# Kernel optimization log

Hardware: AMD Instinct MI355X
Metric: run time of the kernel (lower is better)

Reference implementation:

```python
import jax, jax.numpy as jnp
import numpy as np

K_NEIGS = 3
M_PROB = 1.0
EPS = 1e-12


def _gen_G_single(ft):
    """Build normalized hypergraph Laplacian G [N,N] from node coords ft [N,3].

    Mirrors construct_H_with_KNN (is_probH=True, m_prob=1) + generate_G_from_H
    from the HGNN reference code: per-center KNN hyperedges with probabilistic
    incidence exp(-d^2/(m_prob*avg_d)^2), then G = Dv^-1/2 H De^-1 H^T Dv^-1/2.
    """
    N = ft.shape[0]
    # squared pairwise Euclidean distances [N,N]
    sq_norm = jnp.sum(ft * ft, axis=1)
    sq = jnp.maximum(sq_norm[:, None] + sq_norm[None, :] - 2.0 * ft @ ft.T, 0.0)
    dist = jnp.sqrt(sq + EPS)
    avg_dis = jnp.mean(dist, axis=1)  # per-center mean distance [N]
    # K nearest neighbors per center (self is always included: sq[c,c]=0)
    neg_sq, idx = jax.lax.top_k(-sq, K_NEIGS)  # [N,K]
    # prob incidence: exp(-d^2 / (m_prob*avg)^2); neg_sq = -d^2
    vals = jnp.exp(neg_sq / (M_PROB * avg_dis[:, None]) ** 2)  # [N,K]
    # H[node, edge]: column c holds the K neighbors of center c
    H = jnp.zeros((N, N), ft.dtype).at[idx, jnp.arange(N)[:, None]].set(vals)
    de = jnp.sum(H, axis=0)              # edge degrees [N]
    dv = jnp.sum(H, axis=1)              # vertex degrees [N]
    inv_de = 1.0 / de
    dv2 = dv ** -0.5
    HW = H * inv_de[None, :]
    G = (dv2[:, None] * (HW @ H.T)) * dv2[None, :]
    return G


def reference(x, W1, b1, Wc, bc):
    # gen_G: per-batch hypergraph G [B,N,N]
    G = jax.vmap(_gen_G_single)(x)
    # HGNN_conv with both args = G: out = G @ (G @ W1 + b1)  -> [B,N,H1]
    f = jnp.matmul(G, jnp.matmul(G, W1) + b1)
    # max-pool over nodes, then classifier
    f = jnp.max(f, axis=1)               # [B,H1]
    return f @ Wc + bc                   # [B,class_num]


def setup_inputs() -> dict:
    key = jax.random.key(0)
    k1, k2, k3, k4, k5 = jax.random.split(key, 5)
    B, N, H1, C = 4, 2048, 128, 8
    x = jax.random.normal(k1, (B, N, 3), dtype=jnp.float32)
    W1 = jax.random.normal(k2, (N, H1), dtype=jnp.float32) / np.sqrt(N)
    b1 = jax.random.normal(k3, (H1,), dtype=jnp.float32) * 0.01
    Wc = jax.random.normal(k4, (H1, C), dtype=jnp.float32) / np.sqrt(H1)
    bc = jax.random.normal(k5, (C,), dtype=jnp.float32) * 0.01
    return {"x": x, "W1": W1, "b1": b1, "Wc": Wc, "bc": bc}
```

## Files before the change

kernel.cpp:

```cpp
#include <hip/hip_runtime.h>
#include <math.h>

#define NN 2048
#define BB 4
#define HD 128
#define CNUM 8
#define WPB 4
#define PCHUNK 64
#define NCHUNKS (NN / PCHUNK)

typedef unsigned long long u64;

__device__ __forceinline__ u64 pack_key(float sq, int j) {
    return ((u64)__float_as_uint(sq) << 32) | (unsigned)j;
}
__device__ __forceinline__ void ins3(u64 k, u64& k0, u64& k1, u64& k2) {
    u64 a = k  < k2 ? k  : k2;
    u64 b = k0 > a  ? k0 : a;
    k0    = k0 < a  ? k0 : a;
    k2    = k1 > b  ? k1 : b;
    k1    = k1 < b  ? k1 : b;
}

__global__ void k_prep(const float* __restrict__ x, float4* __restrict__ pts) {
    const int t = blockIdx.x * 256 + threadIdx.x;
    const float a = x[3 * t], c = x[3 * t + 1], d = x[3 * t + 2];
    pts[t] = make_float4(a, c, d, a * a + c * c + d * d);
}

__global__ __launch_bounds__(256) void k_dist(
        const float4* __restrict__ pts,
        int* __restrict__ idx, float* __restrict__ vals,
        float* __restrict__ de, float* __restrict__ dv) {
    const int b = blockIdx.y;
    const float4* pb = pts + b * NN;
    const int wave = threadIdx.x >> 6;
    const int lane = threadIdx.x & 63;
    const int i = blockIdx.x * WPB + wave;
    const float4 ci = pb[i];
    u64 k0 = ~0ull, k1 = ~0ull, k2 = ~0ull;
    float dsA = 0.f, dsB = 0.f;
    for (int t = lane; t < NN; t += 256) {
        const float4 pa = pb[t];
        const float4 pv = pb[t + 64];
        const float4 pc = pb[t + 128];
        const float4 pd = pb[t + 192];
        const float qa = fmaxf(ci.w + pa.w - 2.0f * (ci.x * pa.x + ci.y * pa.y + ci.z * pa.z), 0.0f);
        const float qb = fmaxf(ci.w + pv.w - 2.0f * (ci.x * pv.x + ci.y * pv.y + ci.z * pv.z), 0.0f);
        const float qc = fmaxf(ci.w + pc.w - 2.0f * (ci.x * pc.x + ci.y * pc.y + ci.z * pc.z), 0.0f);
        const float qd = fmaxf(ci.w + pd.w - 2.0f * (ci.x * pd.x + ci.y * pd.y + ci.z * pd.z), 0.0f);
        dsA += __builtin_amdgcn_sqrtf(qa + 1e-12f) + __builtin_amdgcn_sqrtf(qc + 1e-12f);
        dsB += __builtin_amdgcn_sqrtf(qb + 1e-12f) + __builtin_amdgcn_sqrtf(qd + 1e-12f);
        ins3(pack_key(qa, t),       k0, k1, k2);
        ins3(pack_key(qb, t + 64),  k0, k1, k2);
        ins3(pack_key(qc, t + 128), k0, k1, k2);
        ins3(pack_key(qd, t + 192), k0, k1, k2);
    }
    float dsum = dsA + dsB;
    for (int off = 32; off > 0; off >>= 1) {
        const u64 o0 = __shfl_xor(k0, off);
        const u64 o1 = __shfl_xor(k1, off);
        const u64 o2 = __shfl_xor(k2, off);
        dsum += __shfl_xor(dsum, off);
        ins3(o0, k0, k1, k2);
        ins3(o1, k0, k1, k2);
        ins3(o2, k0, k1, k2);
    }
    if (lane == 0) {
        const float s0 = __uint_as_float((unsigned)(k0 >> 32));
        const float s1 = __uint_as_float((unsigned)(k1 >> 32));
        const float s2 = __uint_as_float((unsigned)(k2 >> 32));
        const int   i0 = (int)(k0 & 0xffffffffu);
        const int   i1 = (int)(k1 & 0xffffffffu);
        const int   i2 = (int)(k2 & 0xffffffffu);
        const float avg = dsum * (1.0f / NN);
        const float inva2 = 1.0f / (avg * avg);
        const float v0 = expf(-s0 * inva2);
        const float v1 = expf(-s1 * inva2);
        const float v2 = expf(-s2 * inva2);
        const int base = (b * NN + i) * 3;
        idx[base] = i0; idx[base + 1] = i1; idx[base + 2] = i2;
        vals[base] = v0; vals[base + 1] = v1; vals[base + 2] = v2;
        de[b * NN + i] = v0 + v1 + v2;
        atomicAdd(&dv[b * NN + i0], v0);
        atomicAdd(&dv[b * NN + i1], v1);
        atomicAdd(&dv[b * NN + i2], v2);
    }
}

__global__ void k_conv1(const float* __restrict__ W1, const int* __restrict__ idx,
                        const float* __restrict__ vals, const float* __restrict__ de,
                        const float* __restrict__ dv, float* __restrict__ Z1) {
    const int e = blockIdx.x * 2 + (threadIdx.x >> 7);
    const int b = blockIdx.y, h = threadIdx.x & (HD - 1);
    const int base = (b * NN + e) * 3;
    const int j0 = idx[base], j1 = idx[base + 1], j2 = idx[base + 2];
    const float v0 = vals[base], v1 = vals[base + 1], v2 = vals[base + 2];
    const float ide = 1.0f / de[b * NN + e];
    const float g0 = v0 * rsqrtf(dv[b * NN + j0]);
    const float g1 = v1 * rsqrtf(dv[b * NN + j1]);
    const float g2 = v2 * rsqrtf(dv[b * NN + j2]);
    const float y = ide * (g0 * W1[j0 * HD + h] + g1 * W1[j1 * HD + h] + g2 * W1[j2 * HD + h]);
    atomicAdd(&Z1[((size_t)(b * NN + j0)) * HD + h], v0 * y);
    atomicAdd(&Z1[((size_t)(b * NN + j1)) * HD + h], v1 * y);
    atomicAdd(&Z1[((size_t)(b * NN + j2)) * HD + h], v2 * y);
}

__global__ void k_conv2(const float* __restrict__ b1, const int* __restrict__ idx,
                        const float* __restrict__ vals, const float* __restrict__ de,
                        const float* __restrict__ dv, const float* __restrict__ Z1,
                        float* __restrict__ Z2) {
    const int e = blockIdx.x * 2 + (threadIdx.x >> 7);
    const int b = blockIdx.y, h = threadIdx.x & (HD - 1);
    const int base = (b * NN + e) * 3;
    const int j0 = idx[base], j1 = idx[base + 1], j2 = idx[base + 2];
    const float v0 = vals[base], v1 = vals[base + 1], v2 = vals[base + 2];
    const float ide = 1.0f / de[b * NN + e];
    const float bh = b1[h];
    const float d0 = rsqrtf(dv[b * NN + j0]);
    const float d1 = rsqrtf(dv[b * NN + j1]);
    const float d2 = rsqrtf(dv[b * NN + j2]);
    const float f0 = d0 * Z1[((size_t)(b * NN + j0)) * HD + h] + bh;
    const float f1 = d1 * Z1[((size_t)(b * NN + j1)) * HD + h] + bh;
    const float f2 = d2 * Z1[((size_t)(b * NN + j2)) * HD + h] + bh;
    const float y = ide * (v0 * d0 * f0 + v1 * d1 * f1 + v2 * d2 * f2);
    atomicAdd(&Z2[((size_t)(b * NN + j0)) * HD + h], v0 * y);
    atomicAdd(&Z2[((size_t)(b * NN + j1)) * HD + h], v1 * y);
    atomicAdd(&Z2[((size_t)(b * NN + j2)) * HD + h], v2 * y);
}

__global__ void k_pool1(const float* __restrict__ dv, const float* __restrict__ Z2,
                        float* __restrict__ pmax) {
    const int b = blockIdx.x, ch = blockIdx.y, h = threadIdx.x;
    const int v0 = ch * PCHUNK;
    float mx = -INFINITY;
    for (int v = v0; v < v0 + PCHUNK; ++v) {
        const float d2 = rsqrtf(dv[b * NN + v]);
        mx = fmaxf(mx, d2 * Z2[((size_t)(b * NN + v)) * HD + h]);
    }
    pmax[(b * NCHUNKS + ch) * HD + h] = mx;
}

__global__ void k_pool2(const float* __restrict__ Wc, const float* __restrict__ bc,
                        const float* __restrict__ pmax, float* __restrict__ out) {
    __shared__ float smax[HD];
    const int b = blockIdx.x, h = threadIdx.x;
    float mx = -INFINITY;
    for (int c = 0; c < NCHUNKS; ++c)
        mx = fmaxf(mx, pmax[(b * NCHUNKS + c) * HD + h]);
    smax[h] = mx;
    __syncthreads();
    if (h < CNUM) {
        float acc = bc[h];
        for (int q = 0; q < HD; ++q) acc += smax[q] * Wc[q * CNUM + h];
        out[b * CNUM + h] = acc;
    }
}

extern "C" void kernel_launch(void* const* d_in, const int* in_sizes, int n_in,
                              void* d_out, int out_size, void* d_ws, size_t ws_size,
                              hipStream_t stream) {
    const float* x  = (const float*)d_in[0];
    const float* W1 = (const float*)d_in[1];
    const float* b1 = (const float*)d_in[2];
    const float* Wc = (const float*)d_in[3];
    const float* bc = (const float*)d_in[4];
    float* out = (float*)d_out;

    float* ws = (float*)d_ws;
    float* dv   = ws;
    float* Z1   = dv + BB * NN;
    float* Z2   = Z1 + (size_t)BB * NN * HD;
    float* vals = Z2 + (size_t)BB * NN * HD;
    float* de   = vals + BB * NN * 3;
    int*   idx  = (int*)(de + BB * NN);
    float* pmax = (float*)(idx + BB * NN * 3);
    float4* pts = (float4*)(pmax + BB * NCHUNKS * HD);

    hipMemsetAsync(dv, 0, (size_t)(BB * NN) * (1 + 2 * HD) * sizeof(float), stream);

    k_prep<<<BB * NN / 256, 256, 0, stream>>>(x, pts);
    k_dist<<<dim3(NN / WPB, BB), 256, 0, stream>>>(pts, idx, vals, de, dv);
    k_conv1<<<dim3(NN / 2, BB), 256, 0, stream>>>(W1, idx, vals, de, dv, Z1);
    k_conv2<<<dim3(NN / 2, BB), 256, 0, stream>>>(b1, idx, vals, de, dv, Z1, Z2);
    k_pool1<<<dim3(BB, NCHUNKS), HD, 0, stream>>>(dv, Z2, pmax);
    k_pool2<<<BB, HD, 0, stream>>>(Wc, bc, pmax, out);
}
```

Measured before the change: 119.3 us.

## Replace scatter atomics with CSR gather for hypergraph convolutions

Builds a per-batch CSR incidence list (node to hyperedges) with a prefix scan and shared-memory cursors in a new k_csr kernel. Each convolution is split into an edge pass that writes per-edge features and a node pass that gathers them through the CSR, so the large float atomicAdd scatters into Z1/Z2 go away. The 8 MB memset of Z1/Z2 also goes away, and dv^-1/2 is precomputed once. In exchange it adds three kernel launches and a CSR build that runs on only four blocks, and the order in which each node's contributions are summed is no longer fixed.

```diff
diff --git a/kernel.cpp b/kernel.cpp
--- a/kernel.cpp
+++ b/kernel.cpp
@@ -31,7 +31,7 @@
 __global__ __launch_bounds__(256) void k_dist(
         const float4* __restrict__ pts,
         int* __restrict__ idx, float* __restrict__ vals,
-        float* __restrict__ de, float* __restrict__ dv) {
+        float* __restrict__ de, float* __restrict__ dv, int* __restrict__ ecnt) {
     const int b = blockIdx.y;
     const float4* pb = pts + b * NN;
     const int wave = threadIdx.x >> 6;
@@ -85,59 +85,119 @@
         atomicAdd(&dv[b * NN + i0], v0);
         atomicAdd(&dv[b * NN + i1], v1);
         atomicAdd(&dv[b * NN + i2], v2);
-    }
-}
-
-__global__ void k_conv1(const float* __restrict__ W1, const int* __restrict__ idx,
+        atomicAdd(&ecnt[b * NN + i0], 1);
+        atomicAdd(&ecnt[b * NN + i1], 1);
+        atomicAdd(&ecnt[b * NN + i2], 1);
+    }
+}
+
+__global__ __launch_bounds__(256) void k_csr(
+        const float* __restrict__ dv, const int* __restrict__ ecnt,
+        const int* __restrict__ idx, const float* __restrict__ vals,
+        float* __restrict__ dv2, int* __restrict__ offs,
+        int* __restrict__ inc_e, float* __restrict__ inc_v) {
+    __shared__ int part[256];
+    __shared__ int cursor[NN];
+    const int b = blockIdx.x, t = threadIdx.x;
+    for (int v = t; v < NN; v += 256) dv2[b * NN + v] = rsqrtf(dv[b * NN + v]);
+    int c[8];
+    const int g0 = b * NN + t * 8;
+    int s = 0;
+    for (int k = 0; k < 8; ++k) { c[k] = s; s += ecnt[g0 + k]; }
+    part[t] = s;
+    __syncthreads();
+    for (int off = 1; off < 256; off <<= 1) {
+        const int mine = part[t];
+        const int prev = (t >= off) ? part[t - off] : 0;
+        __syncthreads();
+        part[t] = mine + prev;
+        __syncthreads();
+    }
+    const int base = (t > 0) ? part[t - 1] : 0;
+    for (int k = 0; k < 8; ++k) {
+        const int loc = base + c[k];
+        offs[g0 + k] = b * NN * 3 + loc;
+        cursor[t * 8 + k] = loc;
+    }
+    __syncthreads();
+    for (int e = t; e < NN; e += 256) {
+        const int ib = (b * NN + e) * 3;
+        for (int k = 0; k < 3; ++k) {
+            const int j = idx[ib + k];
+            const int slot = atomicAdd(&cursor[j], 1);
+            inc_e[b * NN * 3 + slot] = e;
+            inc_v[b * NN * 3 + slot] = vals[ib + k];
+        }
+    }
+}
+
+__global__ void k_edge1(const float* __restrict__ W1, const int* __restrict__ idx,
                         const float* __restrict__ vals, const float* __restrict__ de,
-                        const float* __restrict__ dv, float* __restrict__ Z1) {
+                        const float* __restrict__ dv2, float* __restrict__ U) {
     const int e = blockIdx.x * 2 + (threadIdx.x >> 7);
     const int b = blockIdx.y, h = threadIdx.x & (HD - 1);
     const int base = (b * NN + e) * 3;
     const int j0 = idx[base], j1 = idx[base + 1], j2 = idx[base + 2];
-    const float v0 = vals[base], v1 = vals[base + 1], v2 = vals[base + 2];
+    const float g0 = vals[base]     * dv2[b * NN + j0];
+    const float g1 = vals[base + 1] * dv2[b * NN + j1];
+    const float g2 = vals[base + 2] * dv2[b * NN + j2];
     const float ide = 1.0f / de[b * NN + e];
-    const float g0 = v0 * rsqrtf(dv[b * NN + j0]);
-    const float g1 = v1 * rsqrtf(dv[b * NN + j1]);
-    const float g2 = v2 * rsqrtf(dv[b * NN + j2]);
-    const float y = ide * (g0 * W1[j0 * HD + h] + g1 * W1[j1 * HD + h] + g2 * W1[j2 * HD + h]);
-    atomicAdd(&Z1[((size_t)(b * NN + j0)) * HD + h], v0 * y);
-    atomicAdd(&Z1[((size_t)(b * NN + j1)) * HD + h], v1 * y);
-    atomicAdd(&Z1[((size_t)(b * NN + j2)) * HD + h], v2 * y);
-}
-
-__global__ void k_conv2(const float* __restrict__ b1, const int* __restrict__ idx,
+    U[((size_t)(b * NN + e)) * HD + h] =
+        ide * (g0 * W1[j0 * HD + h] + g1 * W1[j1 * HD + h] + g2 * W1[j2 * HD + h]);
+}
+
+__global__ void k_node1(const float* __restrict__ U, const int* __restrict__ offs,
+                        const int* __restrict__ inc_e, const float* __restrict__ inc_v,
+                        const float* __restrict__ dv2, const float* __restrict__ b1,
+                        float* __restrict__ M1) {
+    const int v = blockIdx.x * 2 + (threadIdx.x >> 7);
+    const int b = blockIdx.y, h = threadIdx.x & (HD - 1);
+    const int g = b * NN + v;
+    const int start = offs[g];
+    const int end = (v == NN - 1) ? (b + 1) * NN * 3 : offs[g + 1];
+    float acc = 0.f;
+    for (int s = start; s < end; ++s)
+        acc += inc_v[s] * U[((size_t)(b * NN + inc_e[s])) * HD + h];
+    M1[(size_t)g * HD + h] = dv2[g] * acc + b1[h];
+}
+
+__global__ void k_edge2(const float* __restrict__ M1, const int* __restrict__ idx,
                         const float* __restrict__ vals, const float* __restrict__ de,
-                        const float* __restrict__ dv, const float* __restrict__ Z1,
-                        float* __restrict__ Z2) {
+                        const float* __restrict__ dv2, float* __restrict__ U2) {
     const int e = blockIdx.x * 2 + (threadIdx.x >> 7);
     const int b = blockIdx.y, h = threadIdx.x & (HD - 1);
     const int base = (b * NN + e) * 3;
     const int j0 = idx[base], j1 = idx[base + 1], j2 = idx[base + 2];
-    const float v0 = vals[base], v1 = vals[base + 1], v2 = vals[base + 2];
+    const float g0 = vals[base]     * dv2[b * NN + j0];
+    const float g1 = vals[base + 1] * dv2[b * NN + j1];
+    const float g2 = vals[base + 2] * dv2[b * NN + j2];
     const float ide = 1.0f / de[b * NN + e];
-    const float bh = b1[h];
-    const float d0 = rsqrtf(dv[b * NN + j0]);
-    const float d1 = rsqrtf(dv[b * NN + j1]);
-    const float d2 = rsqrtf(dv[b * NN + j2]);
-    const float f0 = d0 * Z1[((size_t)(b * NN + j0)) * HD + h] + bh;
-    const float f1 = d1 * Z1[((size_t)(b * NN + j1)) * HD + h] + bh;
-    const float f2 = d2 * Z1[((size_t)(b * NN + j2)) * HD + h] + bh;
-    const float y = ide * (v0 * d0 * f0 + v1 * d1 * f1 + v2 * d2 * f2);
-    atomicAdd(&Z2[((size_t)(b * NN + j0)) * HD + h], v0 * y);
-    atomicAdd(&Z2[((size_t)(b * NN + j1)) * HD + h], v1 * y);
-    atomicAdd(&Z2[((size_t)(b * NN + j2)) * HD + h], v2 * y);
-}
-
-__global__ void k_pool1(const float* __restrict__ dv, const float* __restrict__ Z2,
-                        float* __restrict__ pmax) {
+    U2[((size_t)(b * NN + e)) * HD + h] =
+        ide * (g0 * M1[((size_t)(b * NN + j0)) * HD + h] +
+               g1 * M1[((size_t)(b * NN + j1)) * HD + h] +
+               g2 * M1[((size_t)(b * NN + j2)) * HD + h]);
+}
+
+__global__ void k_node2(const float* __restrict__ U2, const int* __restrict__ offs,
+                        const int* __restrict__ inc_e, const float* __restrict__ inc_v,
+                        const float* __restrict__ dv2, float* __restrict__ F) {
+    const int v = blockIdx.x * 2 + (threadIdx.x >> 7);
+    const int b = blockIdx.y, h = threadIdx.x & (HD - 1);
+    const int g = b * NN + v;
+    const int start = offs[g];
+    const int end = (v == NN - 1) ? (b + 1) * NN * 3 : offs[g + 1];
+    float acc = 0.f;
+    for (int s = start; s < end; ++s)
+        acc += inc_v[s] * U2[((size_t)(b * NN + inc_e[s])) * HD + h];
+    F[(size_t)g * HD + h] = dv2[g] * acc;
+}
+
+__global__ void k_pool1(const float* __restrict__ F, float* __restrict__ pmax) {
     const int b = blockIdx.x, ch = blockIdx.y, h = threadIdx.x;
     const int v0 = ch * PCHUNK;
     float mx = -INFINITY;
-    for (int v = v0; v < v0 + PCHUNK; ++v) {
-        const float d2 = rsqrtf(dv[b * NN + v]);
-        mx = fmaxf(mx, d2 * Z2[((size_t)(b * NN + v)) * HD + h]);
-    }
+    for (int v = v0; v < v0 + PCHUNK; ++v)
+        mx = fmaxf(mx, F[((size_t)(b * NN + v)) * HD + h]);
     pmax[(b * NCHUNKS + ch) * HD + h] = mx;
 }
 
@@ -168,21 +228,29 @@
     float* out = (float*)d_out;
 
     float* ws = (float*)d_ws;
-    float* dv   = ws;
-    float* Z1   = dv + BB * NN;
-    float* Z2   = Z1 + (size_t)BB * NN * HD;
-    float* vals = Z2 + (size_t)BB * NN * HD;
-    float* de   = vals + BB * NN * 3;
-    int*   idx  = (int*)(de + BB * NN);
-    float* pmax = (float*)(idx + BB * NN * 3);
-    float4* pts = (float4*)(pmax + BB * NCHUNKS * HD);
-
-    hipMemsetAsync(dv, 0, (size_t)(BB * NN) * (1 + 2 * HD) * sizeof(float), stream);
+    float* dv    = ws;
+    int*   ecnt  = (int*)(dv + BB * NN);
+    float* de    = (float*)(ecnt + BB * NN);
+    float* vals  = de + BB * NN;
+    int*   idx   = (int*)(vals + BB * NN * 3);
+    float* dv2   = (float*)(idx + BB * NN * 3);
+    int*   offs  = (int*)(dv2 + BB * NN);
+    int*   inc_e = offs + BB * NN;
+    float* inc_v = (float*)(inc_e + BB * NN * 3);
+    float* U     = inc_v + BB * NN * 3;
+    float* M1    = U + (size_t)BB * NN * HD;
+    float* pmax  = M1 + (size_t)BB * NN * HD;
+    float4* pts  = (float4*)(pmax + BB * NCHUNKS * HD);
+
+    hipMemsetAsync(dv, 0, (size_t)BB * NN * 2 * sizeof(float), stream);
 
     k_prep<<<BB * NN / 256, 256, 0, stream>>>(x, pts);
-    k_dist<<<dim3(NN / WPB, BB), 256, 0, stream>>>(pts, idx, vals, de, dv);
-    k_conv1<<<dim3(NN / 2, BB), 256, 0, stream>>>(W1, idx, vals, de, dv, Z1);
-    k_conv2<<<dim3(NN / 2, BB), 256, 0, stream>>>(b1, idx, vals, de, dv, Z1, Z2);
-    k_pool1<<<dim3(BB, NCHUNKS), HD, 0, stream>>>(dv, Z2, pmax);
+    k_dist<<<dim3(NN / WPB, BB), 256, 0, stream>>>(pts, idx, vals, de, dv, ecnt);
+    k_csr<<<BB, 256, 0, stream>>>(dv, ecnt, idx, vals, dv2, offs, inc_e, inc_v);
+    k_edge1<<<dim3(NN / 2, BB), 256, 0, stream>>>(W1, idx, vals, de, dv2, U);
+    k_node1<<<dim3(NN / 2, BB), 256, 0, stream>>>(U, offs, inc_e, inc_v, dv2, b1, M1);
+    k_edge2<<<dim3(NN / 2, BB), 256, 0, stream>>>(M1, idx, vals, de, dv2, U);
+    k_node2<<<dim3(NN / 2, BB), 256, 0, stream>>>(U, offs, inc_e, inc_v, dv2, M1);
+    k_pool1<<<dim3(BB, NCHUNKS), HD, 0, stream>>>(M1, pmax);
     k_pool2<<<BB, HD, 0, stream>>>(Wc, bc, pmax, out);
 }
```

New measurement: 145.9 us. 1.22x slower.

## Fuse all stages into one cooperative persistent kernel with grid syncs

Applied to the files above, without the earlier changes.

Replaces the memset and six separate kernel launches with a single cooperative kernel of 256 blocks x 512 threads. Zeroing, point prep, KNN/distance, both convolution scatters and the two pooling steps run as phases separated by grid.sync(). The aim is to remove per-launch overhead and the gaps between the small dependent kernels. In exchange it adds grid-wide barrier cost and needs every block to be co-resident on the device.

```diff
diff --git a/kernel.cpp b/kernel.cpp
--- a/kernel.cpp
+++ b/kernel.cpp
@@ -1,13 +1,17 @@
 #include <hip/hip_runtime.h>
+#include <hip/hip_cooperative_groups.h>
 #include <math.h>
+
+namespace cg = cooperative_groups;
 
 #define NN 2048
 #define BB 4
 #define HD 128
 #define CNUM 8
-#define WPB 4
-#define PCHUNK 64
-#define NCHUNKS (NN / PCHUNK)
+#define GB 256
+#define TB 512
+#define NTH (GB * TB)
+#define ZCNT ((BB * NN * (1 + 2 * HD)) / 4)
 
 typedef unsigned long long u64;
 
@@ -22,138 +26,162 @@
     k1    = k1 < b  ? k1 : b;
 }
 
-__global__ void k_prep(const float* __restrict__ x, float4* __restrict__ pts) {
-    const int t = blockIdx.x * 256 + threadIdx.x;
-    const float a = x[3 * t], c = x[3 * t + 1], d = x[3 * t + 2];
-    pts[t] = make_float4(a, c, d, a * a + c * c + d * d);
-}
-
-__global__ __launch_bounds__(256) void k_dist(
-        const float4* __restrict__ pts,
-        int* __restrict__ idx, float* __restrict__ vals,
-        float* __restrict__ de, float* __restrict__ dv) {
-    const int b = blockIdx.y;
-    const float4* pb = pts + b * NN;
-    const int wave = threadIdx.x >> 6;
-    const int lane = threadIdx.x & 63;
-    const int i = blockIdx.x * WPB + wave;
-    const float4 ci = pb[i];
-    u64 k0 = ~0ull, k1 = ~0ull, k2 = ~0ull;
-    float dsA = 0.f, dsB = 0.f;
-    for (int t = lane; t < NN; t += 256) {
-        const float4 pa = pb[t];
-        const float4 pv = pb[t + 64];
-        const float4 pc = pb[t + 128];
-        const float4 pd = pb[t + 192];
-        const float qa = fmaxf(ci.w + pa.w - 2.0f * (ci.x * pa.x + ci.y * pa.y + ci.z * pa.z), 0.0f);
-        const float qb = fmaxf(ci.w + pv.w - 2.0f * (ci.x * pv.x + ci.y * pv.y + ci.z * pv.z), 0.0f);
-        const float qc = fmaxf(ci.w + pc.w - 2.0f * (ci.x * pc.x + ci.y * pc.y + ci.z * pc.z), 0.0f);
-        const float qd = fmaxf(ci.w + pd.w - 2.0f * (ci.x * pd.x + ci.y * pd.y + ci.z * pd.z), 0.0f);
-        dsA += __builtin_amdgcn_sqrtf(qa + 1e-12f) + __builtin_amdgcn_sqrtf(qc + 1e-12f);
-        dsB += __builtin_amdgcn_sqrtf(qb + 1e-12f) + __builtin_amdgcn_sqrtf(qd + 1e-12f);
-        ins3(pack_key(qa, t),       k0, k1, k2);
-        ins3(pack_key(qb, t + 64),  k0, k1, k2);
-        ins3(pack_key(qc, t + 128), k0, k1, k2);
-        ins3(pack_key(qd, t + 192), k0, k1, k2);
-    }
-    float dsum = dsA + dsB;
-    for (int off = 32; off > 0; off >>= 1) {
-        const u64 o0 = __shfl_xor(k0, off);
-        const u64 o1 = __shfl_xor(k1, off);
-        const u64 o2 = __shfl_xor(k2, off);
-        dsum += __shfl_xor(dsum, off);
-        ins3(o0, k0, k1, k2);
-        ins3(o1, k0, k1, k2);
-        ins3(o2, k0, k1, k2);
-    }
-    if (lane == 0) {
-        const float s0 = __uint_as_float((unsigned)(k0 >> 32));
-        const float s1 = __uint_as_float((unsigned)(k1 >> 32));
-        const float s2 = __uint_as_float((unsigned)(k2 >> 32));
-        const int   i0 = (int)(k0 & 0xffffffffu);
-        const int   i1 = (int)(k1 & 0xffffffffu);
-        const int   i2 = (int)(k2 & 0xffffffffu);
-        const float avg = dsum * (1.0f / NN);
-        const float inva2 = 1.0f / (avg * avg);
-        const float v0 = expf(-s0 * inva2);
-        const float v1 = expf(-s1 * inva2);
-        const float v2 = expf(-s2 * inva2);
-        const int base = (b * NN + i) * 3;
-        idx[base] = i0; idx[base + 1] = i1; idx[base + 2] = i2;
-        vals[base] = v0; vals[base + 1] = v1; vals[base + 2] = v2;
-        de[b * NN + i] = v0 + v1 + v2;
-        atomicAdd(&dv[b * NN + i0], v0);
-        atomicAdd(&dv[b * NN + i1], v1);
-        atomicAdd(&dv[b * NN + i2], v2);
-    }
-}
-
-__global__ void k_conv1(const float* __restrict__ W1, const int* __restrict__ idx,
-                        const float* __restrict__ vals, const float* __restrict__ de,
-                        const float* __restrict__ dv, float* __restrict__ Z1) {
-    const int e = blockIdx.x * 2 + (threadIdx.x >> 7);
-    const int b = blockIdx.y, h = threadIdx.x & (HD - 1);
-    const int base = (b * NN + e) * 3;
-    const int j0 = idx[base], j1 = idx[base + 1], j2 = idx[base + 2];
-    const float v0 = vals[base], v1 = vals[base + 1], v2 = vals[base + 2];
-    const float ide = 1.0f / de[b * NN + e];
-    const float g0 = v0 * rsqrtf(dv[b * NN + j0]);
-    const float g1 = v1 * rsqrtf(dv[b * NN + j1]);
-    const float g2 = v2 * rsqrtf(dv[b * NN + j2]);
-    const float y = ide * (g0 * W1[j0 * HD + h] + g1 * W1[j1 * HD + h] + g2 * W1[j2 * HD + h]);
-    atomicAdd(&Z1[((size_t)(b * NN + j0)) * HD + h], v0 * y);
-    atomicAdd(&Z1[((size_t)(b * NN + j1)) * HD + h], v1 * y);
-    atomicAdd(&Z1[((size_t)(b * NN + j2)) * HD + h], v2 * y);
-}
-
-__global__ void k_conv2(const float* __restrict__ b1, const int* __restrict__ idx,
-                        const float* __restrict__ vals, const float* __restrict__ de,
-                        const float* __restrict__ dv, const float* __restrict__ Z1,
-                        float* __restrict__ Z2) {
-    const int e = blockIdx.x * 2 + (threadIdx.x >> 7);
-    const int b = blockIdx.y, h = threadIdx.x & (HD - 1);
-    const int base = (b * NN + e) * 3;
-    const int j0 = idx[base], j1 = idx[base + 1], j2 = idx[base + 2];
-    const float v0 = vals[base], v1 = vals[base + 1], v2 = vals[base + 2];
-    const float ide = 1.0f / de[b * NN + e];
-    const float bh = b1[h];
-    const float d0 = rsqrtf(dv[b * NN + j0]);
-    const float d1 = rsqrtf(dv[b * NN + j1]);
-    const float d2 = rsqrtf(dv[b * NN + j2]);
-    const float f0 = d0 * Z1[((size_t)(b * NN + j0)) * HD + h] + bh;
-    const float f1 = d1 * Z1[((size_t)(b * NN + j1)) * HD + h] + bh;
-    const float f2 = d2 * Z1[((size_t)(b * NN + j2)) * HD + h] + bh;
-    const float y = ide * (v0 * d0 * f0 + v1 * d1 * f1 + v2 * d2 * f2);
-    atomicAdd(&Z2[((size_t)(b * NN + j0)) * HD + h], v0 * y);
-    atomicAdd(&Z2[((size_t)(b * NN + j1)) * HD + h], v1 * y);
-    atomicAdd(&Z2[((size_t)(b * NN + j2)) * HD + h], v2 * y);
-}
-
-__global__ void k_pool1(const float* __restrict__ dv, const float* __restrict__ Z2,
-                        float* __restrict__ pmax) {
-    const int b = blockIdx.x, ch = blockIdx.y, h = threadIdx.x;
-    const int v0 = ch * PCHUNK;
-    float mx = -INFINITY;
-    for (int v = v0; v < v0 + PCHUNK; ++v) {
-        const float d2 = rsqrtf(dv[b * NN + v]);
-        mx = fmaxf(mx, d2 * Z2[((size_t)(b * NN + v)) * HD + h]);
-    }
-    pmax[(b * NCHUNKS + ch) * HD + h] = mx;
-}
-
-__global__ void k_pool2(const float* __restrict__ Wc, const float* __restrict__ bc,
-                        const float* __restrict__ pmax, float* __restrict__ out) {
-    __shared__ float smax[HD];
-    const int b = blockIdx.x, h = threadIdx.x;
-    float mx = -INFINITY;
-    for (int c = 0; c < NCHUNKS; ++c)
-        mx = fmaxf(mx, pmax[(b * NCHUNKS + c) * HD + h]);
-    smax[h] = mx;
-    __syncthreads();
-    if (h < CNUM) {
-        float acc = bc[h];
-        for (int q = 0; q < HD; ++q) acc += smax[q] * Wc[q * CNUM + h];
-        out[b * CNUM + h] = acc;
+__global__ __launch_bounds__(TB, 2) void k_fused(
+        const float* __restrict__ x, const float* __restrict__ W1,
+        const float* __restrict__ b1, const float* __restrict__ Wc,
+        const float* __restrict__ bc, float* __restrict__ out,
+        float4* __restrict__ pts, int* __restrict__ idx,
+        float* __restrict__ vals, float* __restrict__ de,
+        float* __restrict__ dv, float* __restrict__ Z1,
+        float* __restrict__ Z2, float* __restrict__ pmax) {
+    cg::grid_group grid = cg::this_grid();
+    const int tid = threadIdx.x;
+    const int gtid = blockIdx.x * TB + tid;
+
+    {
+        float4* z4 = (float4*)dv;
+        const float4 z = make_float4(0.f, 0.f, 0.f, 0.f);
+        for (int i = gtid; i < ZCNT; i += NTH) z4[i] = z;
+        if (gtid < BB * NN) {
+            const float a = x[3 * gtid], c = x[3 * gtid + 1], d = x[3 * gtid + 2];
+            pts[gtid] = make_float4(a, c, d, a * a + c * c + d * d);
+        }
+    }
+    grid.sync();
+
+    {
+        const int wv = gtid >> 6, lane = gtid & 63;
+        for (int rep = 0; rep < 4; ++rep) {
+            const int c = wv * 4 + rep;
+            const int b = c >> 11, i = c & (NN - 1);
+            const float4* pb = pts + b * NN;
+            const float4 ci = pb[i];
+            u64 k0 = ~0ull, k1 = ~0ull, k2 = ~0ull;
+            float dsA = 0.f, dsB = 0.f;
+            for (int t = lane; t < NN; t += 256) {
+                const float4 pa = pb[t];
+                const float4 pv = pb[t + 64];
+                const float4 pc = pb[t + 128];
+                const float4 pd = pb[t + 192];
+                const float qa = fmaxf(ci.w + pa.w - 2.0f * (ci.x * pa.x + ci.y * pa.y + ci.z * pa.z), 0.0f);
+                const float qb = fmaxf(ci.w + pv.w - 2.0f * (ci.x * pv.x + ci.y * pv.y + ci.z * pv.z), 0.0f);
+                const float qc = fmaxf(ci.w + pc.w - 2.0f * (ci.x * pc.x + ci.y * pc.y + ci.z * pc.z), 0.0f);
+                const float qd = fmaxf(ci.w + pd.w - 2.0f * (ci.x * pd.x + ci.y * pd.y + ci.z * pd.z), 0.0f);
+                dsA += __builtin_amdgcn_sqrtf(qa + 1e-12f) + __builtin_amdgcn_sqrtf(qc + 1e-12f);
+                dsB += __builtin_amdgcn_sqrtf(qb + 1e-12f) + __builtin_amdgcn_sqrtf(qd + 1e-12f);
+                ins3(pack_key(qa, t),       k0, k1, k2);
+                ins3(pack_key(qb, t + 64),  k0, k1, k2);
+                ins3(pack_key(qc, t + 128), k0, k1, k2);
+                ins3(pack_key(qd, t + 192), k0, k1, k2);
+            }
+            float dsum = dsA + dsB;
+            for (int off = 32; off > 0; off >>= 1) {
+                const u64 o0 = __shfl_xor(k0, off);
+                const u64 o1 = __shfl_xor(k1, off);
+                const u64 o2 = __shfl_xor(k2, off);
+                dsum += __shfl_xor(dsum, off);
+                ins3(o0, k0, k1, k2);
+                ins3(o1, k0, k1, k2);
+                ins3(o2, k0, k1, k2);
+            }
+            if (lane == 0) {
+                const float s0 = __uint_as_float((unsigned)(k0 >> 32));
+                const float s1 = __uint_as_float((unsigned)(k1 >> 32));
+                const float s2 = __uint_as_float((unsigned)(k2 >> 32));
+                const int   i0 = (int)(k0 & 0xffffffffu);
+                const int   i1 = (int)(k1 & 0xffffffffu);
+                const int   i2 = (int)(k2 & 0xffffffffu);
+                const float avg = dsum * (1.0f / NN);
+                const float inva2 = 1.0f / (avg * avg);
+                const float v0 = expf(-s0 * inva2);
+                const float v1 = expf(-s1 * inva2);
+                const float v2 = expf(-s2 * inva2);
+                const int base = c * 3;
+                idx[base] = i0; idx[base + 1] = i1; idx[base + 2] = i2;
+                vals[base] = v0; vals[base + 1] = v1; vals[base + 2] = v2;
+                de[c] = v0 + v1 + v2;
+                atomicAdd(&dv[b * NN + i0], v0);
+                atomicAdd(&dv[b * NN + i1], v1);
+                atomicAdd(&dv[b * NN + i2], v2);
+            }
+        }
+    }
+    grid.sync();
+
+    for (int pass = 0; pass < 8; ++pass) {
+        const int gi = pass * NTH + gtid;
+        const int ge = gi >> 7;
+        const int h = gi & (HD - 1);
+        const int b = ge >> 11;
+        const int base = ge * 3;
+        const int j0 = idx[base], j1 = idx[base + 1], j2 = idx[base + 2];
+        const float v0 = vals[base], v1 = vals[base + 1], v2 = vals[base + 2];
+        const float ide = 1.0f / de[ge];
+        const float g0 = v0 * rsqrtf(dv[b * NN + j0]);
+        const float g1 = v1 * rsqrtf(dv[b * NN + j1]);
+        const float g2 = v2 * rsqrtf(dv[b * NN + j2]);
+        const float y = ide * (g0 * W1[j0 * HD + h] + g1 * W1[j1 * HD + h] + g2 * W1[j2 * HD + h]);
+        atomicAdd(&Z1[((size_t)(b * NN + j0)) * HD + h], v0 * y);
+        atomicAdd(&Z1[((size_t)(b * NN + j1)) * HD + h], v1 * y);
+        atomicAdd(&Z1[((size_t)(b * NN + j2)) * HD + h], v2 * y);
+    }
+    grid.sync();
+
+    for (int pass = 0; pass < 8; ++pass) {
+        const int gi = pass * NTH + gtid;
+        const int ge = gi >> 7;
+        const int h = gi & (HD - 1);
+        const int b = ge >> 11;
+        const int base = ge * 3;
+        const int j0 = idx[base], j1 = idx[base + 1], j2 = idx[base + 2];
+        const float v0 = vals[base], v1 = vals[base + 1], v2 = vals[base + 2];
+        const float ide = 1.0f / de[ge];
+        const float bh = b1[h];
+        const float d0 = rsqrtf(dv[b * NN + j0]);
+        const float d1 = rsqrtf(dv[b * NN + j1]);
+        const float d2 = rsqrtf(dv[b * NN + j2]);
+        const float f0 = d0 * Z1[((size_t)(b * NN + j0)) * HD + h] + bh;
+        const float f1 = d1 * Z1[((size_t)(b * NN + j1)) * HD + h] + bh;
+        const float f2 = d2 * Z1[((size_t)(b * NN + j2)) * HD + h] + bh;
+        const float y = ide * (v0 * d0 * f0 + v1 * d1 * f1 + v2 * d2 * f2);
+        atomicAdd(&Z2[((size_t)(b * NN + j0)) * HD + h], v0 * y);
+        atomicAdd(&Z2[((size_t)(b * NN + j1)) * HD + h], v1 * y);
+        atomicAdd(&Z2[((size_t)(b * NN + j2)) * HD + h], v2 * y);
+    }
+    grid.sync();
+
+    __shared__ float sm[4][HD];
+    {
+        const int b = blockIdx.x >> 6, ch = blockIdx.x & 63;
+        const int h = tid & (HD - 1), sub = tid >> 7;
+        float mx = -INFINITY;
+        for (int n = 0; n < 8; ++n) {
+            const int g = b * NN + ch * 32 + sub * 8 + n;
+            mx = fmaxf(mx, rsqrtf(dv[g]) * Z2[(size_t)g * HD + h]);
+        }
+        sm[sub][h] = mx;
+        __syncthreads();
+        if (sub == 0)
+            pmax[(b * 64 + ch) * HD + h] =
+                fmaxf(fmaxf(sm[0][h], sm[1][h]), fmaxf(sm[2][h], sm[3][h]));
+    }
+    grid.sync();
+
+    if (blockIdx.x < BB) {
+        const int b = blockIdx.x;
+        __shared__ float smax[HD];
+        if (tid < HD) {
+            float mx = -INFINITY;
+            for (int c = 0; c < 64; ++c)
+                mx = fmaxf(mx, pmax[(b * 64 + c) * HD + tid]);
+            smax[tid] = mx;
+        }
+        __syncthreads();
+        if (tid < CNUM) {
+            float acc = bc[tid];
+            for (int q = 0; q < HD; ++q) acc += smax[q] * Wc[q * CNUM + tid];
+            out[b * CNUM + tid] = acc;
+        }
     }
 }
 
@@ -168,21 +196,17 @@
     float* out = (float*)d_out;
 
     float* ws = (float*)d_ws;
-    float* dv   = ws;
-    float* Z1   = dv + BB * NN;
-    float* Z2   = Z1 + (size_t)BB * NN * HD;
-    float* vals = Z2 + (size_t)BB * NN * HD;
-    float* de   = vals + BB * NN * 3;
-    int*   idx  = (int*)(de + BB * NN);
-    float* pmax = (float*)(idx + BB * NN * 3);
-    float4* pts = (float4*)(pmax + BB * NCHUNKS * HD);
-
-    hipMemsetAsync(dv, 0, (size_t)(BB * NN) * (1 + 2 * HD) * sizeof(float), stream);
-
-    k_prep<<<BB * NN / 256, 256, 0, stream>>>(x, pts);
-    k_dist<<<dim3(NN / WPB, BB), 256, 0, stream>>>(pts, idx, vals, de, dv);
-    k_conv1<<<dim3(NN / 2, BB), 256, 0, stream>>>(W1, idx, vals, de, dv, Z1);
-    k_conv2<<<dim3(NN / 2, BB), 256, 0, stream>>>(b1, idx, vals, de, dv, Z1, Z2);
-    k_pool1<<<dim3(BB, NCHUNKS), HD, 0, stream>>>(dv, Z2, pmax);
-    k_pool2<<<BB, HD, 0, stream>>>(Wc, bc, pmax, out);
-}
+    float*  dv   = ws;
+    float*  Z1   = dv + BB * NN;
+    float*  Z2   = Z1 + (size_t)BB * NN * HD;
+    float*  vals = Z2 + (size_t)BB * NN * HD;
+    float*  de   = vals + BB * NN * 3;
+    int*    idx  = (int*)(de + BB * NN);
+    float*  pmax = (float*)(idx + BB * NN * 3);
+    float4* pts  = (float4*)(pmax + BB * 64 * HD);
+
+    void* args[] = { (void*)&x, (void*)&W1, (void*)&b1, (void*)&Wc, (void*)&bc,
+                     (void*)&out, (void*)&pts, (void*)&idx, (void*)&vals,
+                     (void*)&de, (void*)&dv, (void*)&Z1, (void*)&Z2, (void*)&pmax };
+    hipLaunchCooperativeKernel((void*)k_fused, dim3(GB), dim3(TB), args, 0, stream);
+}
```

New measurement: 279.8 us. 135% more time.

## Fuse memset into prep kernel, prefetch points in k_dist, merge pooling kernels

Applied to the files above, without the earlier changes.

Replaces the hipMemsetAsync with zeroing done inside a new k_init kernel that also packs the points. k_dist now software-prefetches the next batch of points into registers while computing the current one. The two pooling kernels are merged into one 1024-thread block per batch, with a shared-memory max reduction. This removes two launches and the memset. The fused pool runs on only 4 blocks, so it has much less parallelism for reading Z2.

```diff
diff --git a/kernel.cpp b/kernel.cpp
--- a/kernel.cpp
+++ b/kernel.cpp
@@ -6,8 +6,7 @@
 #define HD 128
 #define CNUM 8
 #define WPB 4
-#define PCHUNK 64
-#define NCHUNKS (NN / PCHUNK)
+#define ZF4 ((BB * NN * (1 + 2 * HD)) / 4)
 
 typedef unsigned long long u64;
 
@@ -22,10 +21,17 @@
     k1    = k1 < b  ? k1 : b;
 }
 
-__global__ void k_prep(const float* __restrict__ x, float4* __restrict__ pts) {
-    const int t = blockIdx.x * 256 + threadIdx.x;
-    const float a = x[3 * t], c = x[3 * t + 1], d = x[3 * t + 2];
-    pts[t] = make_float4(a, c, d, a * a + c * c + d * d);
+__global__ __launch_bounds__(256) void k_init(const float* __restrict__ x,
+                                              float* __restrict__ zbase,
+                                              float4* __restrict__ pts) {
+    const int gtid = blockIdx.x * 256 + threadIdx.x;
+    float4* z4 = (float4*)zbase;
+    const float4 z = make_float4(0.f, 0.f, 0.f, 0.f);
+    for (int i = gtid; i < ZF4; i += 65536) z4[i] = z;
+    if (gtid < BB * NN) {
+        const float a = x[3 * gtid], c = x[3 * gtid + 1], d = x[3 * gtid + 2];
+        pts[gtid] = make_float4(a, c, d, a * a + c * c + d * d);
+    }
 }
 
 __global__ __launch_bounds__(256) void k_dist(
@@ -40,15 +46,19 @@
     const float4 ci = pb[i];
     u64 k0 = ~0ull, k1 = ~0ull, k2 = ~0ull;
     float dsA = 0.f, dsB = 0.f;
+    float4 pa = pb[lane], pv = pb[lane + 64], pc = pb[lane + 128], pd = pb[lane + 192];
     for (int t = lane; t < NN; t += 256) {
-        const float4 pa = pb[t];
-        const float4 pv = pb[t + 64];
-        const float4 pc = pb[t + 128];
-        const float4 pd = pb[t + 192];
-        const float qa = fmaxf(ci.w + pa.w - 2.0f * (ci.x * pa.x + ci.y * pa.y + ci.z * pa.z), 0.0f);
-        const float qb = fmaxf(ci.w + pv.w - 2.0f * (ci.x * pv.x + ci.y * pv.y + ci.z * pv.z), 0.0f);
-        const float qc = fmaxf(ci.w + pc.w - 2.0f * (ci.x * pc.x + ci.y * pc.y + ci.z * pc.z), 0.0f);
-        const float qd = fmaxf(ci.w + pd.w - 2.0f * (ci.x * pd.x + ci.y * pd.y + ci.z * pd.z), 0.0f);
+        const float4 ca = pa, cv = pv, cc = pc, cd = pd;
+        if (t + 256 < NN) {
+            pa = pb[t + 256];
+            pv = pb[t + 320];
+            pc = pb[t + 384];
+            pd = pb[t + 448];
+        }
+        const float qa = fmaxf(ci.w + ca.w - 2.0f * (ci.x * ca.x + ci.y * ca.y + ci.z * ca.z), 0.0f);
+        const float qb = fmaxf(ci.w + cv.w - 2.0f * (ci.x * cv.x + ci.y * cv.y + ci.z * cv.z), 0.0f);
+        const float qc = fmaxf(ci.w + cc.w - 2.0f * (ci.x * cc.x + ci.y * cc.y + ci.z * cc.z), 0.0f);
+        const float qd = fmaxf(ci.w + cd.w - 2.0f * (ci.x * cd.x + ci.y * cd.y + ci.z * cd.z), 0.0f);
         dsA += __builtin_amdgcn_sqrtf(qa + 1e-12f) + __builtin_amdgcn_sqrtf(qc + 1e-12f);
         dsB += __builtin_amdgcn_sqrtf(qb + 1e-12f) + __builtin_amdgcn_sqrtf(qd + 1e-12f);
         ins3(pack_key(qa, t),       k0, k1, k2);
@@ -129,31 +139,32 @@
     atomicAdd(&Z2[((size_t)(b * NN + j2)) * HD + h], v2 * y);
 }
 
-__global__ void k_pool1(const float* __restrict__ dv, const float* __restrict__ Z2,
-                        float* __restrict__ pmax) {
-    const int b = blockIdx.x, ch = blockIdx.y, h = threadIdx.x;
-    const int v0 = ch * PCHUNK;
+__global__ __launch_bounds__(1024) void k_pool(
+        const float* __restrict__ Wc, const float* __restrict__ bc,
+        const float* __restrict__ dv, const float* __restrict__ Z2,
+        float* __restrict__ out) {
+    __shared__ float sm[8][HD];
+    __shared__ float smax[HD];
+    const int b = blockIdx.x;
+    const int h = threadIdx.x & (HD - 1);
+    const int q = threadIdx.x >> 7;
     float mx = -INFINITY;
-    for (int v = v0; v < v0 + PCHUNK; ++v) {
-        const float d2 = rsqrtf(dv[b * NN + v]);
-        mx = fmaxf(mx, d2 * Z2[((size_t)(b * NN + v)) * HD + h]);
+    for (int n = 0; n < NN / 8; ++n) {
+        const int g = b * NN + q * (NN / 8) + n;
+        mx = fmaxf(mx, rsqrtf(dv[g]) * Z2[(size_t)g * HD + h]);
     }
-    pmax[(b * NCHUNKS + ch) * HD + h] = mx;
-}
-
-__global__ void k_pool2(const float* __restrict__ Wc, const float* __restrict__ bc,
-                        const float* __restrict__ pmax, float* __restrict__ out) {
-    __shared__ float smax[HD];
-    const int b = blockIdx.x, h = threadIdx.x;
-    float mx = -INFINITY;
-    for (int c = 0; c < NCHUNKS; ++c)
-        mx = fmaxf(mx, pmax[(b * NCHUNKS + c) * HD + h]);
-    smax[h] = mx;
+    sm[q][h] = mx;
     __syncthreads();
-    if (h < CNUM) {
-        float acc = bc[h];
-        for (int q = 0; q < HD; ++q) acc += smax[q] * Wc[q * CNUM + h];
-        out[b * CNUM + h] = acc;
+    if (threadIdx.x < HD) {
+        float m = sm[0][h];
+        for (int p = 1; p < 8; ++p) m = fmaxf(m, sm[p][h]);
+        smax[h] = m;
+    }
+    __syncthreads();
+    if (threadIdx.x < CNUM) {
+        float acc = bc[threadIdx.x];
+        for (int k = 0; k < HD; ++k) acc += smax[k] * Wc[k * CNUM + threadIdx.x];
+        out[b * CNUM + threadIdx.x] = acc;
     }
 }
 
@@ -168,21 +179,17 @@
     float* out = (float*)d_out;
 
     float* ws = (float*)d_ws;
-    float* dv   = ws;
-    float* Z1   = dv + BB * NN;
-    float* Z2   = Z1 + (size_t)BB * NN * HD;
-    float* vals = Z2 + (size_t)BB * NN * HD;
-    float* de   = vals + BB * NN * 3;
-    int*   idx  = (int*)(de + BB * NN);
-    float* pmax = (float*)(idx + BB * NN * 3);
-    float4* pts = (float4*)(pmax + BB * NCHUNKS * HD);
+    float*  dv   = ws;
+    float*  Z1   = dv + BB * NN;
+    float*  Z2   = Z1 + (size_t)BB * NN * HD;
+    float*  vals = Z2 + (size_t)BB * NN * HD;
+    float*  de   = vals + BB * NN * 3;
+    int*    idx  = (int*)(de + BB * NN);
+    float4* pts  = (float4*)(idx + BB * NN * 3);
 
-    hipMemsetAsync(dv, 0, (size_t)(BB * NN) * (1 + 2 * HD) * sizeof(float), stream);
-
-    k_prep<<<BB * NN / 256, 256, 0, stream>>>(x, pts);
+    k_init<<<256, 256, 0, stream>>>(x, dv, pts);
     k_dist<<<dim3(NN / WPB, BB), 256, 0, stream>>>(pts, idx, vals, de, dv);
     k_conv1<<<dim3(NN / 2, BB), 256, 0, stream>>>(W1, idx, vals, de, dv, Z1);
     k_conv2<<<dim3(NN / 2, BB), 256, 0, stream>>>(b1, idx, vals, de, dv, Z1, Z2);
-    k_pool1<<<dim3(BB, NCHUNKS), HD, 0, stream>>>(dv, Z2, pmax);
-    k_pool2<<<BB, HD, 0, stream>>>(Wc, bc, pmax, out);
+    k_pool<<<BB, 1024, 0, stream>>>(Wc, bc, dv, Z2, out);
 }
```

Result: slower. 134.4 us (+12.7%).
